# Performance work log

Hardware: AMD Instinct MI355X
Metric: run time of the kernel (lower is better)

Reference implementation:

```python
import jax, jax.numpy as jnp
import numpy as np

N = 50000       # nodes
E = 800000      # directed edges (before self-loops)
IN = 128        # in_channels
H = 8           # heads
C = 32          # hidden_channels (per head)
OUT = 4         # out_channels
NS_ATT = 0.2    # PyG GATConv attention leaky-relu slope
NS_ACT = 0.01   # model activation leaky-relu slope
EPS = 1e-5      # BatchNorm eps


def setup_inputs() -> dict:
    key = jax.random.key(0)
    ks = jax.random.split(key, 18)
    s = 0.05
    return {
        "x": jax.random.normal(ks[0], (N, IN), jnp.float32),
        "edge_index": jax.random.randint(ks[1], (2, E), 0, N, dtype=jnp.int32),
        # layer 1: GATConv(IN -> C, heads=H, concat)
        "W1": jax.random.normal(ks[2], (IN, H * C), jnp.float32) * s,
        "as1": jax.random.normal(ks[3], (H, C), jnp.float32) * s,
        "ad1": jax.random.normal(ks[4], (H, C), jnp.float32) * s,
        "b1": jnp.zeros((H * C,), jnp.float32),
        "g1": jnp.ones((H * C,), jnp.float32),
        "be1": jnp.zeros((H * C,), jnp.float32),
        # middle layer: GATConv(H*C -> C, heads=H, concat) + BN + residual
        "W2": jax.random.normal(ks[5], (H * C, H * C), jnp.float32) * s,
        "as2": jax.random.normal(ks[6], (H, C), jnp.float32) * s,
        "ad2": jax.random.normal(ks[7], (H, C), jnp.float32) * s,
        "b2": jnp.zeros((H * C,), jnp.float32),
        "g2": jnp.ones((H * C,), jnp.float32),
        "be2": jnp.zeros((H * C,), jnp.float32),
        # final layer: GATConv(H*C -> OUT, heads=1, concat=False)
        "W3": jax.random.normal(ks[8], (H * C, OUT), jnp.float32) * s,
        "as3": jax.random.normal(ks[9], (1, OUT), jnp.float32) * s,
        "ad3": jax.random.normal(ks[10], (1, OUT), jnp.float32) * s,
        "b3": jnp.zeros((OUT,), jnp.float32),
    }


def _lrelu(x, slope):
    return jnp.where(x >= 0, x, slope * x)


def _gat_conv(x, src, dst, W, a_src, a_dst, bias, heads, ch, concat):
    # PyG GATConv: h = x @ W per head; edge logit = LReLU(a_src.h_j + a_dst.h_i)
    n = x.shape[0]
    h = (x @ W).reshape(n, heads, ch)                      # [N,H,C]
    al_s = jnp.sum(h * a_src, axis=-1)                     # [N,H]
    al_d = jnp.sum(h * a_dst, axis=-1)                     # [N,H]
    logits = _lrelu(al_s[src] + al_d[dst], NS_ATT)         # [E,H]
    # segment softmax over edges grouped by destination node
    m = jax.ops.segment_max(logits, dst, num_segments=n)   # [N,H]
    e = jnp.exp(logits - m[dst])
    denom = jax.ops.segment_sum(e, dst, num_segments=n)
    alpha = e / (denom[dst] + 1e-16)                       # [E,H]
    out = jax.ops.segment_sum(alpha[:, :, None] * h[src], dst, num_segments=n)  # [N,H,C]
    if concat:
        return out.reshape(n, heads * ch) + bias
    return out.mean(axis=1) + bias


def _bn(x, gamma, beta):
    mu = jnp.mean(x, axis=0)
    var = jnp.mean((x - mu) ** 2, axis=0)
    return (x - mu) * jax.lax.rsqrt(var + EPS) * gamma + beta


def reference(x, edge_index, W1, as1, ad1, b1, g1, be1,
              W2, as2, ad2, b2, g2, be2, W3, as3, ad3, b3):
    n = x.shape[0]
    loops = jnp.arange(n, dtype=edge_index.dtype)          # self-loops (PyG default)
    src = jnp.concatenate([edge_index[0], loops])
    dst = jnp.concatenate([edge_index[1], loops])
    h = _lrelu(_bn(_gat_conv(x, src, dst, W1, as1, ad1, b1, H, C, True), g1, be1), NS_ACT)
    residual = h
    h = _lrelu(_bn(_gat_conv(h, src, dst, W2, as2, ad2, b2, H, C, True), g2, be2), NS_ACT)
    h = h + residual
    return _gat_conv(h, src, dst, W3, as3, ad3, b3, 1, OUT, False)
```

## Files before the change

### kernel.cpp

```cpp
#include <hip/hip_runtime.h>

typedef __attribute__((ext_vector_type(8))) short bf16x8;
typedef __attribute__((ext_vector_type(4))) float f32x4;

__device__ __forceinline__ float lrelu(float x, float s) { return x >= 0.f ? x : s * x; }
__device__ __forceinline__ float b2f(unsigned short u) {
  union { unsigned int i; float f; } v; v.i = ((unsigned int)u) << 16; return v.f;
}
__device__ __forceinline__ float b2f_lo(unsigned int u) {
  union { unsigned int i; float f; } v; v.i = u << 16; return v.f;
}
__device__ __forceinline__ float b2f_hi(unsigned int u) {
  union { unsigned int i; float f; } v; v.i = u & 0xffff0000u; return v.f;
}
__device__ __forceinline__ unsigned short f2b(float f) {
  union { float f; unsigned int i; } v; v.f = f;
  unsigned int r = v.i + 0x7fffu + ((v.i >> 16) & 1u);
  return (unsigned short)(r >> 16);
}
__device__ __forceinline__ unsigned int fbits(float f) {
  union { float f; unsigned int i; } v; v.f = f; return v.i;
}
__device__ __forceinline__ float bitsf(unsigned int u) {
  union { unsigned int i; float f; } v; v.i = u; return v.f;
}

__global__ __launch_bounds__(256) void k_hist(const int* __restrict__ dst, int e,
                                              int* __restrict__ cnt) {
  int i = blockIdx.x * 256 + threadIdx.x;
  if (i < e) atomicAdd(&cnt[dst[i]], 1);
}

__global__ __launch_bounds__(256) void k_bsum(const int* __restrict__ cnt,
                                              int* __restrict__ bsum, int n) {
  const int base = blockIdx.x * 1024;
  const int t = threadIdx.x;
  int s = 0;
#pragma unroll
  for (int i = 0; i < 4; ++i) {
    int idx = base + t + i * 256;
    if (idx < n) s += cnt[idx] + 1;
  }
#pragma unroll
  for (int off = 1; off < 64; off <<= 1) s += __shfl_xor(s, off);
  __shared__ int ws[4];
  const int lane = t & 63, w = t >> 6;
  if (lane == 0) ws[w] = s;
  __syncthreads();
  if (t == 0) bsum[blockIdx.x] = ws[0] + ws[1] + ws[2] + ws[3];
}

__global__ __launch_bounds__(256) void k_scanl(const int* __restrict__ cnt,
                                               const int* __restrict__ bsum,
                                               int* __restrict__ ptr,
                                               int* __restrict__ fill, int n, int B) {
  __shared__ int ws[4];
  __shared__ int bo;
  const int t = threadIdx.x;
  if (t < 64) {
    int v = t < B ? bsum[t] : 0;
    int incl = v;
#pragma unroll
    for (int off = 1; off < 64; off <<= 1) {
      int u = __shfl_up(incl, off);
      if (t >= off) incl += u;
    }
    if (t == blockIdx.x) bo = incl - v;
    if (blockIdx.x == 0 && t == 63) ptr[n] = incl;
  }
  const int base = blockIdx.x * 1024 + t * 4;
  int v0 = base + 0 < n ? cnt[base + 0] + 1 : 0;
  int v1 = base + 1 < n ? cnt[base + 1] + 1 : 0;
  int v2 = base + 2 < n ? cnt[base + 2] + 1 : 0;
  int v3 = base + 3 < n ? cnt[base + 3] + 1 : 0;
  const int tsum = v0 + v1 + v2 + v3;
  const int lane = t & 63, w = t >> 6;
  int incl = tsum;
#pragma unroll
  for (int off = 1; off < 64; off <<= 1) {
    int u = __shfl_up(incl, off);
    if (lane >= off) incl += u;
  }
  if (lane == 63) ws[w] = incl;
  __syncthreads();
  int excl = bo + incl - tsum;
  for (int i = 0; i < w; ++i) excl += ws[i];
  if (base + 0 < n) { ptr[base + 0] = excl; fill[base + 0] = excl; }
  excl += v0;
  if (base + 1 < n) { ptr[base + 1] = excl; fill[base + 1] = excl; }
  excl += v1;
  if (base + 2 < n) { ptr[base + 2] = excl; fill[base + 2] = excl; }
  excl += v2;
  if (base + 3 < n) { ptr[base + 3] = excl; fill[base + 3] = excl; }
}

__global__ __launch_bounds__(256) void k_scatter(const int* __restrict__ srce,
                                                 const int* __restrict__ dste,
                                                 int e, int n,
                                                 int* __restrict__ fill,
                                                 int* __restrict__ srcs) {
  int i = blockIdx.x * 256 + threadIdx.x;
  if (i < e) {
    int pos = atomicAdd(&fill[dste[i]], 1);
    srcs[pos] = srce[i];
  } else if (i < e + n) {
    int v = i - e;
    int pos = atomicAdd(&fill[v], 1);
    srcs[pos] = v;
  }
}

__global__ __launch_bounds__(256) void k_prep(int* __restrict__ cnt, int n,
                                              const float* __restrict__ x,
                                              unsigned short* __restrict__ xb,
                                              const float* __restrict__ W1,
                                              unsigned short* __restrict__ w1t,
                                              const float* __restrict__ W2,
                                              unsigned short* __restrict__ w2t, int n4) {
  int i = blockIdx.x * 256 + threadIdx.x;
  if (i < n) {
    cnt[i] = 0;
  }
  if (i < n) return;
  i -= n;
  if (i < n4) {
    float4 v = ((const float4*)x)[i];
    ushort4 o;
    o.x = f2b(v.x); o.y = f2b(v.y); o.z = f2b(v.z); o.w = f2b(v.w);
    ((ushort4*)xb)[i] = o;
    return;
  }
  i -= n4;
  if (i < 256 * 128) {
    int nn = i / 128, k = i - nn * 128;
    w1t[i] = f2b(W1[(size_t)k * 256 + nn]);
    return;
  }
  i -= 256 * 128;
  if (i < 256 * 256) {
    int nn = i / 256, k = i - nn * 256;
    w2t[i] = f2b(W2[(size_t)k * 256 + nn]);
  }
}

__global__ __launch_bounds__(256) void k_mfma(const unsigned short* __restrict__ A,
                                              const unsigned short* __restrict__ BT,
                                              unsigned short* __restrict__ C,
                                              const float* __restrict__ as_,
                                              const float* __restrict__ ad_,
                                              float* __restrict__ als,
                                              float* __restrict__ ald,
                                              int M, int Nn, int K) {
  __shared__ unsigned int Asu[128 * 20];
  __shared__ unsigned int Bsu[128 * 20];
  const int tid = threadIdx.x;
  const int bm = blockIdx.x * 128, bn = blockIdx.y * 128;
  const int w = tid >> 6, lane = tid & 63;
  const int wm = w >> 1, wn = w & 1;
  const int l16 = lane & 15, lg = lane >> 4;
  f32x4 acc[4][4] = {};
  for (int k0 = 0; k0 < K; k0 += 32) {
#pragma unroll
    for (int rep = 0; rep < 2; ++rep) {
      int ci = tid + rep * 256;
      int row = ci >> 2, cg = ci & 3;
      int ar = bm + row;
      ar = ar < M ? ar : M - 1;
      uint4 av = *(const uint4*)(A + (size_t)ar * K + k0 + cg * 8);
      *(uint4*)&Asu[row * 20 + cg * 4] = av;
      uint4 bv = *(const uint4*)(BT + (size_t)(bn + row) * K + k0 + cg * 8);
      *(uint4*)&Bsu[row * 20 + cg * 4] = bv;
    }
    __syncthreads();
    bf16x8 aF[4], bF[4];
#pragma unroll
    for (int mi = 0; mi < 4; ++mi)
      aF[mi] = *(const bf16x8*)&Asu[(wm * 64 + mi * 16 + l16) * 20 + lg * 4];
#pragma unroll
    for (int ni = 0; ni < 4; ++ni)
      bF[ni] = *(const bf16x8*)&Bsu[(wn * 64 + ni * 16 + l16) * 20 + lg * 4];
#pragma unroll
    for (int mi = 0; mi < 4; ++mi)
#pragma unroll
      for (int ni = 0; ni < 4; ++ni)
        acc[mi][ni] =
            __builtin_amdgcn_mfma_f32_16x16x32_bf16(aF[mi], bF[ni], acc[mi][ni], 0, 0, 0);
    __syncthreads();
  }
  float asv[4], adv[4];
#pragma unroll
  for (int ni = 0; ni < 4; ++ni) {
    int gcol = bn + wn * 64 + ni * 16 + l16;
    asv[ni] = as_[gcol];
    adv[ni] = ad_[gcol];
  }
  const int hb = (bn >> 5) + wn * 2;
#pragma unroll
  for (int mi = 0; mi < 4; ++mi) {
#pragma unroll
    for (int r = 0; r < 4; ++r) {
      int grow = bm + wm * 64 + mi * 16 + lg * 4 + r;
      bool ok = grow < M;
      if (ok) {
#pragma unroll
        for (int ni = 0; ni < 4; ++ni) {
          int gcol = bn + wn * 64 + ni * 16 + l16;
          C[(size_t)grow * Nn + gcol] = f2b(acc[mi][ni][r]);
        }
      }
      float ps0 = acc[mi][0][r] * asv[0] + acc[mi][1][r] * asv[1];
      float ps1 = acc[mi][2][r] * asv[2] + acc[mi][3][r] * asv[3];
      float pd0 = acc[mi][0][r] * adv[0] + acc[mi][1][r] * adv[1];
      float pd1 = acc[mi][2][r] * adv[2] + acc[mi][3][r] * adv[3];
#pragma unroll
      for (int off = 1; off < 16; off <<= 1) {
        ps0 += __shfl_xor(ps0, off);
        ps1 += __shfl_xor(ps1, off);
        pd0 += __shfl_xor(pd0, off);
        pd1 += __shfl_xor(pd1, off);
      }
      if (ok && l16 == 0) {
        *(float2*)(als + (size_t)grow * 8 + hb) = make_float2(ps0, ps1);
        *(float2*)(ald + (size_t)grow * 8 + hb) = make_float2(pd0, pd1);
      }
    }
  }
}

__global__ __launch_bounds__(256) void k_agg(const unsigned short* __restrict__ h,
                                             const float* __restrict__ als,
                                             const float* __restrict__ ald,
                                             const int* __restrict__ ptr,
                                             const int* __restrict__ srcs,
                                             const float* __restrict__ bias,
                                             unsigned short* __restrict__ out, int n) {
  int wid = (blockIdx.x * 256 + threadIdx.x) >> 6;
  int lane = threadIdx.x & 63;
  if (wid >= n) return;
  const int beg = ptr[wid], end = ptr[wid + 1];
  const int L = lane & 15;
  const int e = lane >> 4;
  const int hh = L >> 1;
  const float adh = ald[(size_t)wid * 8 + hh];
  float s = 0.f;
  float a0 = 0, a1 = 0, a2 = 0, a3 = 0, a4 = 0, a5 = 0, a6 = 0, a7 = 0;
  float a8 = 0, a9 = 0, aA = 0, aB = 0, aC = 0, aD = 0, aE = 0, aF = 0;
  for (int j = beg + e; j < end; j += 8) {
    const int jB = j + 4;
    const bool vB = jB < end;
    int sA = srcs[j];
    int sB = vB ? srcs[jB] : sA;
    const uint4* hpA = (const uint4*)(h + (size_t)sA * 256 + L * 16);
    const uint4* hpB = (const uint4*)(h + (size_t)sB * 256 + L * 16);
    uint4 cA0 = hpA[0];
    uint4 cA1 = hpA[1];
    uint4 cB0 = hpB[0];
    uint4 cB1 = hpB[1];
    float alsA = als[(size_t)sA * 8 + hh];
    float alsB = als[(size_t)sB * 8 + hh];
    float wtA = __expf(lrelu(alsA + adh, 0.2f));
    s += wtA;
    a0 += wtA * b2f_lo(cA0.x); a1 += wtA * b2f_hi(cA0.x);
    a2 += wtA * b2f_lo(cA0.y); a3 += wtA * b2f_hi(cA0.y);
    a4 += wtA * b2f_lo(cA0.z); a5 += wtA * b2f_hi(cA0.z);
    a6 += wtA * b2f_lo(cA0.w); a7 += wtA * b2f_hi(cA0.w);
    a8 += wtA * b2f_lo(cA1.x); a9 += wtA * b2f_hi(cA1.x);
    aA += wtA * b2f_lo(cA1.y); aB += wtA * b2f_hi(cA1.y);
    aC += wtA * b2f_lo(cA1.z); aD += wtA * b2f_hi(cA1.z);
    aE += wtA * b2f_lo(cA1.w); aF += wtA * b2f_hi(cA1.w);
    float wtB = vB ? __expf(lrelu(alsB + adh, 0.2f)) : 0.f;
    s += wtB;
    a0 += wtB * b2f_lo(cB0.x); a1 += wtB * b2f_hi(cB0.x);
    a2 += wtB * b2f_lo(cB0.y); a3 += wtB * b2f_hi(cB0.y);
    a4 += wtB * b2f_lo(cB0.z); a5 += wtB * b2f_hi(cB0.z);
    a6 += wtB * b2f_lo(cB0.w); a7 += wtB * b2f_hi(cB0.w);
    a8 += wtB * b2f_lo(cB1.x); a9 += wtB * b2f_hi(cB1.x);
    aA += wtB * b2f_lo(cB1.y); aB += wtB * b2f_hi(cB1.y);
    aC += wtB * b2f_lo(cB1.z); aD += wtB * b2f_hi(cB1.z);
    aE += wtB * b2f_lo(cB1.w); aF += wtB * b2f_hi(cB1.w);
  }
  a0 += __shfl_xor(a0, 16); a0 += __shfl_xor(a0, 32);
  a1 += __shfl_xor(a1, 16); a1 += __shfl_xor(a1, 32);
  a2 += __shfl_xor(a2, 16); a2 += __shfl_xor(a2, 32);
  a3 += __shfl_xor(a3, 16); a3 += __shfl_xor(a3, 32);
  a4 += __shfl_xor(a4, 16); a4 += __shfl_xor(a4, 32);
  a5 += __shfl_xor(a5, 16); a5 += __shfl_xor(a5, 32);
  a6 += __shfl_xor(a6, 16); a6 += __shfl_xor(a6, 32);
  a7 += __shfl_xor(a7, 16); a7 += __shfl_xor(a7, 32);
  a8 += __shfl_xor(a8, 16); a8 += __shfl_xor(a8, 32);
  a9 += __shfl_xor(a9, 16); a9 += __shfl_xor(a9, 32);
  aA += __shfl_xor(aA, 16); aA += __shfl_xor(aA, 32);
  aB += __shfl_xor(aB, 16); aB += __shfl_xor(aB, 32);
  aC += __shfl_xor(aC, 16); aC += __shfl_xor(aC, 32);
  aD += __shfl_xor(aD, 16); aD += __shfl_xor(aD, 32);
  aE += __shfl_xor(aE, 16); aE += __shfl_xor(aE, 32);
  aF += __shfl_xor(aF, 16); aF += __shfl_xor(aF, 32);
  s += __shfl_xor(s, 16); s += __shfl_xor(s, 32);
  const float inv = 1.f / (s + 1e-16f);
  if (e == 0) {
    const float4* bp = (const float4*)(bias + L * 16);
    float4 b0 = bp[0], b1 = bp[1], b2 = bp[2], b3 = bp[3];
    uint4 o0, o1;
    o0.x = (unsigned int)f2b(a0 * inv + b0.x) | ((unsigned int)f2b(a1 * inv + b0.y) << 16);
    o0.y = (unsigned int)f2b(a2 * inv + b0.z) | ((unsigned int)f2b(a3 * inv + b0.w) << 16);
    o0.z = (unsigned int)f2b(a4 * inv + b1.x) | ((unsigned int)f2b(a5 * inv + b1.y) << 16);
    o0.w = (unsigned int)f2b(a6 * inv + b1.z) | ((unsigned int)f2b(a7 * inv + b1.w) << 16);
    o1.x = (unsigned int)f2b(a8 * inv + b2.x) | ((unsigned int)f2b(a9 * inv + b2.y) << 16);
    o1.y = (unsigned int)f2b(aA * inv + b2.z) | ((unsigned int)f2b(aB * inv + b2.w) << 16);
    o1.z = (unsigned int)f2b(aC * inv + b3.x) | ((unsigned int)f2b(aD * inv + b3.y) << 16);
    o1.w = (unsigned int)f2b(aE * inv + b3.z) | ((unsigned int)f2b(aF * inv + b3.w) << 16);
    uint4* op = (uint4*)(out + (size_t)wid * 256 + L * 16);
    op[0] = o0;
    op[1] = o1;
  }
}

__global__ __launch_bounds__(256) void k_bnp1(const unsigned short* __restrict__ x,
                                              float* __restrict__ partial, int n) {
  const int t = threadIdx.x;
  const int q = t & 63;
  const int rsub = t >> 6;
  float s0 = 0, s1 = 0, s2 = 0, s3 = 0, q0 = 0, q1 = 0, q2 = 0, q3 = 0;
  int r = blockIdx.x * 4 + rsub;
  for (; r + 6144 < n; r += 8192) {
    ushort4 va = *(const ushort4*)(x + (size_t)r * 256 + q * 4);
    ushort4 vb = *(const ushort4*)(x + (size_t)(r + 2048) * 256 + q * 4);
    ushort4 vc = *(const ushort4*)(x + (size_t)(r + 4096) * 256 + q * 4);
    ushort4 vd = *(const ushort4*)(x + (size_t)(r + 6144) * 256 + q * 4);
    float f;
    f = b2f(va.x); s0 += f; q0 += f * f;
    f = b2f(va.y); s1 += f; q1 += f * f;
    f = b2f(va.z); s2 += f; q2 += f * f;
    f = b2f(va.w); s3 += f; q3 += f * f;
    f = b2f(vb.x); s0 += f; q0 += f * f;
    f = b2f(vb.y); s1 += f; q1 += f * f;
    f = b2f(vb.z); s2 += f; q2 += f * f;
    f = b2f(vb.w); s3 += f; q3 += f * f;
    f = b2f(vc.x); s0 += f; q0 += f * f;
    f = b2f(vc.y); s1 += f; q1 += f * f;
    f = b2f(vc.z); s2 += f; q2 += f * f;
    f = b2f(vc.w); s3 += f; q3 += f * f;
    f = b2f(vd.x); s0 += f; q0 += f * f;
    f = b2f(vd.y); s1 += f; q1 += f * f;
    f = b2f(vd.z); s2 += f; q2 += f * f;
    f = b2f(vd.w); s3 += f; q3 += f * f;
  }
  for (; r < n; r += 2048) {
    ushort4 v = *(const ushort4*)(x + (size_t)r * 256 + q * 4);
    float f;
    f = b2f(v.x); s0 += f; q0 += f * f;
    f = b2f(v.y); s1 += f; q1 += f * f;
    f = b2f(v.z); s2 += f; q2 += f * f;
    f = b2f(v.w); s3 += f; q3 += f * f;
  }
  __shared__ float ls[4][512];
  ls[rsub][q * 4 + 0] = s0; ls[rsub][q * 4 + 1] = s1;
  ls[rsub][q * 4 + 2] = s2; ls[rsub][q * 4 + 3] = s3;
  ls[rsub][256 + q * 4 + 0] = q0; ls[rsub][256 + q * 4 + 1] = q1;
  ls[rsub][256 + q * 4 + 2] = q2; ls[rsub][256 + q * 4 + 3] = q3;
  __syncthreads();
  float a = ls[0][t] + ls[1][t] + ls[2][t] + ls[3][t];
  float b = ls[0][256 + t] + ls[1][256 + t] + ls[2][256 + t] + ls[3][256 + t];
  partial[blockIdx.x * 512 + t] = a;
  partial[blockIdx.x * 512 + 256 + t] = b;
}

__global__ __launch_bounds__(256) void k_bnp2(const float* __restrict__ partial,
                                              const float* __restrict__ ga,
                                              const float* __restrict__ be,
                                              float* __restrict__ ss, float invn) {
  const int c = blockIdx.x * 4 + (threadIdx.x >> 6);
  const int lane = threadIdx.x & 63;
  float s = 0.f, qq = 0.f;
#pragma unroll
  for (int k = 0; k < 8; ++k) {
    int b = lane + k * 64;
    s += partial[(size_t)b * 512 + c];
    qq += partial[(size_t)b * 512 + 256 + c];
  }
#pragma unroll
  for (int off = 1; off < 64; off <<= 1) {
    s += __shfl_xor(s, off);
    qq += __shfl_xor(qq, off);
  }
  if (lane == 0) {
    float mu = s * invn;
    float var = qq * invn - mu * mu;
    float sc = ga[c] * rsqrtf(var + 1e-5f);
    ss[c] = sc;
    ss[256 + c] = be[c] - mu * sc;
  }
}

__global__ __launch_bounds__(256) void k_bnact(const unsigned short* __restrict__ x,
                                               const float* __restrict__ ss,
                                               unsigned short* __restrict__ out, int n) {
  const int tot4 = n * 64;
  for (int t = blockIdx.x * 256 + threadIdx.x; t < tot4; t += gridDim.x * 256) {
    int i0 = t * 4;
    int c = i0 & 255;
    ushort4 xu = *(const ushort4*)(x + i0);
    float4 scv = *(const float4*)(ss + c);
    float4 shv = *(const float4*)(ss + 256 + c);
    float t0 = b2f(xu.x) * scv.x + shv.x;
    float t1 = b2f(xu.y) * scv.y + shv.y;
    float t2 = b2f(xu.z) * scv.z + shv.z;
    float t3 = b2f(xu.w) * scv.w + shv.w;
    float o0 = fmaxf(t0, 0.01f * t0);
    float o1 = fmaxf(t1, 0.01f * t1);
    float o2 = fmaxf(t2, 0.01f * t2);
    float o3 = fmaxf(t3, 0.01f * t3);
    ushort4 ob;
    ob.x = f2b(o0); ob.y = f2b(o1); ob.z = f2b(o2); ob.w = f2b(o3);
    *(ushort4*)(out + i0) = ob;
  }
}

__global__ __launch_bounds__(256) void k_bnact3(const unsigned short* __restrict__ x,
                                                const float* __restrict__ ss,
                                                const unsigned short* __restrict__ res,
                                                const float* __restrict__ W3,
                                                const float* __restrict__ as3,
                                                const float* __restrict__ ad3,
                                                uint4* __restrict__ h3p, int n) {
  int wid = (blockIdx.x * 256 + threadIdx.x) >> 6;
  int lane = threadIdx.x & 63;
  if (wid >= n) return;
  const int c = lane * 4;
  ushort4 xu = *(const ushort4*)(x + (size_t)wid * 256 + c);
  ushort4 rv = *(const ushort4*)(res + (size_t)wid * 256 + c);
  float4 scv = *(const float4*)(ss + c);
  float4 shv = *(const float4*)(ss + 256 + c);
  float t0 = b2f(xu.x) * scv.x + shv.x;
  float t1 = b2f(xu.y) * scv.y + shv.y;
  float t2 = b2f(xu.z) * scv.z + shv.z;
  float t3 = b2f(xu.w) * scv.w + shv.w;
  float o0 = fmaxf(t0, 0.01f * t0) + b2f(rv.x);
  float o1 = fmaxf(t1, 0.01f * t1) + b2f(rv.y);
  float o2 = fmaxf(t2, 0.01f * t2) + b2f(rv.z);
  float o3 = fmaxf(t3, 0.01f * t3) + b2f(rv.w);
  const float4* Wp = (const float4*)W3 + lane * 4;
  float4 w0 = Wp[0], w1 = Wp[1], w2 = Wp[2], w3 = Wp[3];
  float a0 = o0 * w0.x + o1 * w1.x + o2 * w2.x + o3 * w3.x;
  float a1 = o0 * w0.y + o1 * w1.y + o2 * w2.y + o3 * w3.y;
  float a2 = o0 * w0.z + o1 * w1.z + o2 * w2.z + o3 * w3.z;
  float a3 = o0 * w0.w + o1 * w1.w + o2 * w2.w + o3 * w3.w;
#pragma unroll
  for (int off = 1; off < 64; off <<= 1) {
    a0 += __shfl_xor(a0, off);
    a1 += __shfl_xor(a1, off);
    a2 += __shfl_xor(a2, off);
    a3 += __shfl_xor(a3, off);
  }
  if (lane == 0) {
    float als3v = a0 * as3[0] + a1 * as3[1] + a2 * as3[2] + a3 * as3[3];
    float ald3v = a0 * ad3[0] + a1 * ad3[1] + a2 * ad3[2] + a3 * ad3[3];
    uint4 pv;
    pv.x = (unsigned int)f2b(a0) | ((unsigned int)f2b(a1) << 16);
    pv.y = (unsigned int)f2b(a2) | ((unsigned int)f2b(a3) << 16);
    pv.z = fbits(als3v);
    pv.w = fbits(ald3v);
    h3p[wid] = pv;
  }
}

__global__ __launch_bounds__(256) void k_agg3(const uint4* __restrict__ h3p,
                                              const int* __restrict__ ptr,
                                              const int* __restrict__ srcs,
                                              const float* __restrict__ b3,
                                              float* __restrict__ out, int n) {
  int wid = (blockIdx.x * 256 + threadIdx.x) >> 6;
  int lane = threadIdx.x & 63;
  if (wid >= n) return;
  const int beg = ptr[wid], end = ptr[wid + 1];
  const float aldh = bitsf(h3p[wid].w);
  float s = 0.f, a0 = 0.f, a1 = 0.f, a2 = 0.f, a3 = 0.f;
  for (int j = beg + lane; j < end; j += 64) {
    uint4 v = h3p[srcs[j]];
    float wgt = __expf(lrelu(bitsf(v.z) + aldh, 0.2f));
    s += wgt;
    a0 += wgt * b2f_lo(v.x);
    a1 += wgt * b2f_hi(v.x);
    a2 += wgt * b2f_lo(v.y);
    a3 += wgt * b2f_hi(v.y);
  }
#pragma unroll
  for (int off = 1; off < 64; off <<= 1) {
    s += __shfl_xor(s, off);
    a0 += __shfl_xor(a0, off);
    a1 += __shfl_xor(a1, off);
    a2 += __shfl_xor(a2, off);
    a3 += __shfl_xor(a3, off);
  }
  if (lane == 0) {
    float inv = 1.f / (s + 1e-16f);
    out[(size_t)wid * 4 + 0] = a0 * inv + b3[0];
    out[(size_t)wid * 4 + 1] = a1 * inv + b3[1];
    out[(size_t)wid * 4 + 2] = a2 * inv + b3[2];
    out[(size_t)wid * 4 + 3] = a3 * inv + b3[3];
  }
}

extern "C" void kernel_launch(void* const* d_in, const int* in_sizes, int n_in,
                              void* d_out, int out_size, void* d_ws, size_t ws_size,
                              hipStream_t stream) {
  const float* x   = (const float*)d_in[0];
  const int*   ei  = (const int*)d_in[1];
  const float* W1  = (const float*)d_in[2];
  const float* as1 = (const float*)d_in[3];
  const float* ad1 = (const float*)d_in[4];
  const float* b1  = (const float*)d_in[5];
  const float* ga1 = (const float*)d_in[6];
  const float* be1 = (const float*)d_in[7];
  const float* W2  = (const float*)d_in[8];
  const float* as2 = (const float*)d_in[9];
  const float* ad2 = (const float*)d_in[10];
  const float* b2  = (const float*)d_in[11];
  const float* ga2 = (const float*)d_in[12];
  const float* be2 = (const float*)d_in[13];
  const float* W3  = (const float*)d_in[14];
  const float* as3 = (const float*)d_in[15];
  const float* ad3 = (const float*)d_in[16];
  const float* b3  = (const float*)d_in[17];

  const int N = in_sizes[0] / 128;
  const int E = in_sizes[1] / 2;
  const int ET = E + N;
  float* out = (float*)d_out;

  char* w = (char*)d_ws;
  auto alloc = [&](size_t bytes) -> void* {
    void* p = (void*)w;
    w += (bytes + 255) & ~(size_t)255;
    return p;
  };
  int* ptr              = (int*)alloc((size_t)(N + 1) * 4);
  int* fill             = (int*)alloc((size_t)N * 4);
  int* cnt              = (int*)alloc((size_t)N * 4);
  int* bsum             = (int*)alloc(64 * 4);
  int* srcs             = (int*)alloc((size_t)ET * 4);
  unsigned short* hbuf  = (unsigned short*)alloc((size_t)N * 256 * 2);
  unsigned short* aggb  = (unsigned short*)alloc((size_t)N * 256 * 2);
  unsigned short* a1b   = (unsigned short*)alloc((size_t)N * 256 * 2);
  unsigned short* xb    = (unsigned short*)alloc((size_t)N * 128 * 2);
  unsigned short* w1t   = (unsigned short*)alloc(256 * 128 * 2);
  unsigned short* w2t   = (unsigned short*)alloc(256 * 256 * 2);
  float* als            = (float*)alloc((size_t)N * 8 * 4);
  float* ald            = (float*)alloc((size_t)N * 8 * 4);
  uint4* h3p            = (uint4*)alloc((size_t)N * 16);
  float* partial        = (float*)alloc(512 * 512 * 4);
  float* ss             = (float*)alloc(1024 * 4);

  const int* esrc = ei;
  const int* edst = ei + E;
  const float invn = 1.f / (float)N;

  const int n4 = N * 32;
  const int prep_tot = N + n4 + 256 * 128 + 256 * 256;
  k_prep<<<(prep_tot + 255) / 256, 256, 0, stream>>>(cnt, N, x, xb, W1, w1t, W2, w2t, n4);

  const int B = (N + 1023) / 1024;
  k_hist<<<(E + 255) / 256, 256, 0, stream>>>(edst, E, cnt);
  k_bsum<<<B, 256, 0, stream>>>(cnt, bsum, N);
  k_scanl<<<B, 256, 0, stream>>>(cnt, bsum, ptr, fill, N, B);
  k_scatter<<<(ET + 255) / 256, 256, 0, stream>>>(esrc, edst, E, N, fill, srcs);

  const dim3 gemm_grid((N + 127) / 128, 2);
  const int wblocks = (N + 3) / 4;

  k_mfma<<<gemm_grid, 256, 0, stream>>>(xb, w1t, hbuf, as1, ad1, als, ald, N, 256, 128);
  k_agg<<<wblocks, 256, 0, stream>>>(hbuf, als, ald, ptr, srcs, b1, aggb, N);
  k_bnp1<<<512, 256, 0, stream>>>(aggb, partial, N);
  k_bnp2<<<64, 256, 0, stream>>>(partial, ga1, be1, ss, invn);
  k_bnact<<<2048, 256, 0, stream>>>(aggb, ss, a1b, N);

  k_mfma<<<gemm_grid, 256, 0, stream>>>(a1b, w2t, hbuf, as2, ad2, als, ald, N, 256, 256);
  k_agg<<<wblocks, 256, 0, stream>>>(hbuf, als, ald, ptr, srcs, b2, aggb, N);
  k_bnp1<<<512, 256, 0, stream>>>(aggb, partial, N);
  k_bnp2<<<64, 256, 0, stream>>>(partial, ga2, be2, ss + 512, invn);
  k_bnact3<<<wblocks, 256, 0, stream>>>(aggb, ss + 512, a1b, W3, as3, ad3, h3p, N);

  k_agg3<<<wblocks, 256, 0, stream>>>(h3p, ptr, srcs, b3, out, N);
}
```

Baseline: 374.5 us.

## Restructure GAT aggregation to per-head persistent waves with 16 edges in flight

Rewrites the aggregation kernel so that each block handles a single attention head, and a wave loops persistently over destination nodes on a fixed 2048-block grid. Each lane covers 8 channels of one head, and 16 edges are processed in parallel per wave, in place of 4 edge groups covering all 256 channels. This is meant to raise memory-level parallelism for the gathered neighbour rows and to cut per-lane register pressure. The cost is that srcs/ptr/ald are re-read once per head, and each gather is only 64 bytes per edge per head. Separately, the edge-scatter writes and the srcs loads now use nontemporal hints, and the prep kernel's divisions become shifts and masks.

```diff
diff --git a/kernel.cpp b/kernel.cpp
--- a/kernel.cpp
+++ b/kernel.cpp
@@ -102,11 +102,11 @@
   int i = blockIdx.x * 256 + threadIdx.x;
   if (i < e) {
     int pos = atomicAdd(&fill[dste[i]], 1);
-    srcs[pos] = srce[i];
+    __builtin_nontemporal_store(srce[i], &srcs[pos]);
   } else if (i < e + n) {
     int v = i - e;
     int pos = atomicAdd(&fill[v], 1);
-    srcs[pos] = v;
+    __builtin_nontemporal_store(v, &srcs[pos]);
   }
 }
 
@@ -120,8 +120,8 @@
   int i = blockIdx.x * 256 + threadIdx.x;
   if (i < n) {
     cnt[i] = 0;
-  }
-  if (i < n) return;
+    return;
+  }
   i -= n;
   if (i < n4) {
     float4 v = ((const float4*)x)[i];
@@ -132,13 +132,13 @@
   }
   i -= n4;
   if (i < 256 * 128) {
-    int nn = i / 128, k = i - nn * 128;
+    int nn = i >> 7, k = i & 127;
     w1t[i] = f2b(W1[(size_t)k * 256 + nn]);
     return;
   }
   i -= 256 * 128;
   if (i < 256 * 256) {
-    int nn = i / 256, k = i - nn * 256;
+    int nn = i >> 8, k = i & 255;
     w2t[i] = f2b(W2[(size_t)k * 256 + nn]);
   }
 }
@@ -234,84 +234,52 @@
                                              const int* __restrict__ srcs,
                                              const float* __restrict__ bias,
                                              unsigned short* __restrict__ out, int n) {
-  int wid = (blockIdx.x * 256 + threadIdx.x) >> 6;
-  int lane = threadIdx.x & 63;
-  if (wid >= n) return;
-  const int beg = ptr[wid], end = ptr[wid + 1];
-  const int L = lane & 15;
-  const int e = lane >> 4;
-  const int hh = L >> 1;
-  const float adh = ald[(size_t)wid * 8 + hh];
-  float s = 0.f;
-  float a0 = 0, a1 = 0, a2 = 0, a3 = 0, a4 = 0, a5 = 0, a6 = 0, a7 = 0;
-  float a8 = 0, a9 = 0, aA = 0, aB = 0, aC = 0, aD = 0, aE = 0, aF = 0;
-  for (int j = beg + e; j < end; j += 8) {
-    const int jB = j + 4;
-    const bool vB = jB < end;
-    int sA = srcs[j];
-    int sB = vB ? srcs[jB] : sA;
-    const uint4* hpA = (const uint4*)(h + (size_t)sA * 256 + L * 16);
-    const uint4* hpB = (const uint4*)(h + (size_t)sB * 256 + L * 16);
-    uint4 cA0 = hpA[0];
-    uint4 cA1 = hpA[1];
-    uint4 cB0 = hpB[0];
-    uint4 cB1 = hpB[1];
-    float alsA = als[(size_t)sA * 8 + hh];
-    float alsB = als[(size_t)sB * 8 + hh];
-    float wtA = __expf(lrelu(alsA + adh, 0.2f));
-    s += wtA;
-    a0 += wtA * b2f_lo(cA0.x); a1 += wtA * b2f_hi(cA0.x);
-    a2 += wtA * b2f_lo(cA0.y); a3 += wtA * b2f_hi(cA0.y);
-    a4 += wtA * b2f_lo(cA0.z); a5 += wtA * b2f_hi(cA0.z);
-    a6 += wtA * b2f_lo(cA0.w); a7 += wtA * b2f_hi(cA0.w);
-    a8 += wtA * b2f_lo(cA1.x); a9 += wtA * b2f_hi(cA1.x);
-    aA += wtA * b2f_lo(cA1.y); aB += wtA * b2f_hi(cA1.y);
-    aC += wtA * b2f_lo(cA1.z); aD += wtA * b2f_hi(cA1.z);
-    aE += wtA * b2f_lo(cA1.w); aF += wtA * b2f_hi(cA1.w);
-    float wtB = vB ? __expf(lrelu(alsB + adh, 0.2f)) : 0.f;
-    s += wtB;
-    a0 += wtB * b2f_lo(cB0.x); a1 += wtB * b2f_hi(cB0.x);
-    a2 += wtB * b2f_lo(cB0.y); a3 += wtB * b2f_hi(cB0.y);
-    a4 += wtB * b2f_lo(cB0.z); a5 += wtB * b2f_hi(cB0.z);
-    a6 += wtB * b2f_lo(cB0.w); a7 += wtB * b2f_hi(cB0.w);
-    a8 += wtB * b2f_lo(cB1.x); a9 += wtB * b2f_hi(cB1.x);
-    aA += wtB * b2f_lo(cB1.y); aB += wtB * b2f_hi(cB1.y);
-    aC += wtB * b2f_lo(cB1.z); aD += wtB * b2f_hi(cB1.z);
-    aE += wtB * b2f_lo(cB1.w); aF += wtB * b2f_hi(cB1.w);
-  }
-  a0 += __shfl_xor(a0, 16); a0 += __shfl_xor(a0, 32);
-  a1 += __shfl_xor(a1, 16); a1 += __shfl_xor(a1, 32);
-  a2 += __shfl_xor(a2, 16); a2 += __shfl_xor(a2, 32);
-  a3 += __shfl_xor(a3, 16); a3 += __shfl_xor(a3, 32);
-  a4 += __shfl_xor(a4, 16); a4 += __shfl_xor(a4, 32);
-  a5 += __shfl_xor(a5, 16); a5 += __shfl_xor(a5, 32);
-  a6 += __shfl_xor(a6, 16); a6 += __shfl_xor(a6, 32);
-  a7 += __shfl_xor(a7, 16); a7 += __shfl_xor(a7, 32);
-  a8 += __shfl_xor(a8, 16); a8 += __shfl_xor(a8, 32);
-  a9 += __shfl_xor(a9, 16); a9 += __shfl_xor(a9, 32);
-  aA += __shfl_xor(aA, 16); aA += __shfl_xor(aA, 32);
-  aB += __shfl_xor(aB, 16); aB += __shfl_xor(aB, 32);
-  aC += __shfl_xor(aC, 16); aC += __shfl_xor(aC, 32);
-  aD += __shfl_xor(aD, 16); aD += __shfl_xor(aD, 32);
-  aE += __shfl_xor(aE, 16); aE += __shfl_xor(aE, 32);
-  aF += __shfl_xor(aF, 16); aF += __shfl_xor(aF, 32);
-  s += __shfl_xor(s, 16); s += __shfl_xor(s, 32);
-  const float inv = 1.f / (s + 1e-16f);
-  if (e == 0) {
-    const float4* bp = (const float4*)(bias + L * 16);
-    float4 b0 = bp[0], b1 = bp[1], b2 = bp[2], b3 = bp[3];
-    uint4 o0, o1;
-    o0.x = (unsigned int)f2b(a0 * inv + b0.x) | ((unsigned int)f2b(a1 * inv + b0.y) << 16);
-    o0.y = (unsigned int)f2b(a2 * inv + b0.z) | ((unsigned int)f2b(a3 * inv + b0.w) << 16);
-    o0.z = (unsigned int)f2b(a4 * inv + b1.x) | ((unsigned int)f2b(a5 * inv + b1.y) << 16);
-    o0.w = (unsigned int)f2b(a6 * inv + b1.z) | ((unsigned int)f2b(a7 * inv + b1.w) << 16);
-    o1.x = (unsigned int)f2b(a8 * inv + b2.x) | ((unsigned int)f2b(a9 * inv + b2.y) << 16);
-    o1.y = (unsigned int)f2b(aA * inv + b2.z) | ((unsigned int)f2b(aB * inv + b2.w) << 16);
-    o1.z = (unsigned int)f2b(aC * inv + b3.x) | ((unsigned int)f2b(aD * inv + b3.y) << 16);
-    o1.w = (unsigned int)f2b(aE * inv + b3.z) | ((unsigned int)f2b(aF * inv + b3.w) << 16);
-    uint4* op = (uint4*)(out + (size_t)wid * 256 + L * 16);
-    op[0] = o0;
-    op[1] = o1;
+  const int head = blockIdx.x & 7;
+  const int wv = threadIdx.x >> 6;
+  const int lane = threadIdx.x & 63;
+  const int e = lane >> 2;
+  const int l = lane & 3;
+  const int ch = head * 32 + l * 8;
+  const float4 bv0 = *(const float4*)(bias + ch);
+  const float4 bv1 = *(const float4*)(bias + ch + 4);
+  const int dst0 = (blockIdx.x >> 3) * 4 + wv;
+  const int dstep = (gridDim.x >> 3) * 4;
+  for (int dst = dst0; dst < n; dst += dstep) {
+    const int beg = ptr[dst], end = ptr[dst + 1];
+    const float adh = ald[(size_t)dst * 8 + head];
+    float s = 0.f;
+    float a0 = 0, a1 = 0, a2 = 0, a3 = 0, a4 = 0, a5 = 0, a6 = 0, a7 = 0;
+    for (int j = beg + e; j < end; j += 16) {
+      int src = __builtin_nontemporal_load(&srcs[j]);
+      float wt = __expf(lrelu(als[(size_t)src * 8 + head] + adh, 0.2f));
+      uint4 hv = *(const uint4*)(h + (size_t)src * 256 + ch);
+      s += wt;
+      a0 += wt * b2f_lo(hv.x); a1 += wt * b2f_hi(hv.x);
+      a2 += wt * b2f_lo(hv.y); a3 += wt * b2f_hi(hv.y);
+      a4 += wt * b2f_lo(hv.z); a5 += wt * b2f_hi(hv.z);
+      a6 += wt * b2f_lo(hv.w); a7 += wt * b2f_hi(hv.w);
+    }
+#pragma unroll
+    for (int off = 4; off < 64; off <<= 1) {
+      s  += __shfl_xor(s, off);
+      a0 += __shfl_xor(a0, off);
+      a1 += __shfl_xor(a1, off);
+      a2 += __shfl_xor(a2, off);
+      a3 += __shfl_xor(a3, off);
+      a4 += __shfl_xor(a4, off);
+      a5 += __shfl_xor(a5, off);
+      a6 += __shfl_xor(a6, off);
+      a7 += __shfl_xor(a7, off);
+    }
+    if (e == 0) {
+      float inv = 1.f / (s + 1e-16f);
+      uint4 o;
+      o.x = (unsigned int)f2b(a0 * inv + bv0.x) | ((unsigned int)f2b(a1 * inv + bv0.y) << 16);
+      o.y = (unsigned int)f2b(a2 * inv + bv0.z) | ((unsigned int)f2b(a3 * inv + bv0.w) << 16);
+      o.z = (unsigned int)f2b(a4 * inv + bv1.x) | ((unsigned int)f2b(a5 * inv + bv1.y) << 16);
+      o.w = (unsigned int)f2b(a6 * inv + bv1.z) | ((unsigned int)f2b(a7 * inv + bv1.w) << 16);
+      *(uint4*)(out + (size_t)dst * 256 + ch) = o;
+    }
   }
 }
 
@@ -567,15 +535,16 @@
 
   const dim3 gemm_grid((N + 127) / 128, 2);
   const int wblocks = (N + 3) / 4;
+  const int agg_grid = 2048;
 
   k_mfma<<<gemm_grid, 256, 0, stream>>>(xb, w1t, hbuf, as1, ad1, als, ald, N, 256, 128);
-  k_agg<<<wblocks, 256, 0, stream>>>(hbuf, als, ald, ptr, srcs, b1, aggb, N);
+  k_agg<<<agg_grid, 256, 0, stream>>>(hbuf, als, ald, ptr, srcs, b1, aggb, N);
   k_bnp1<<<512, 256, 0, stream>>>(aggb, partial, N);
   k_bnp2<<<64, 256, 0, stream>>>(partial, ga1, be1, ss, invn);
   k_bnact<<<2048, 256, 0, stream>>>(aggb, ss, a1b, N);
 
   k_mfma<<<gemm_grid, 256, 0, stream>>>(a1b, w2t, hbuf, as2, ad2, als, ald, N, 256, 256);
-  k_agg<<<wblocks, 256, 0, stream>>>(hbuf, als, ald, ptr, srcs, b2, aggb, N);
+  k_agg<<<agg_grid, 256, 0, stream>>>(hbuf, als, ald, ptr, srcs, b2, aggb, N);
   k_bnp1<<<512, 256, 0, stream>>>(aggb, partial, N);
   k_bnp2<<<64, 256, 0, stream>>>(partial, ga2, be2, ss + 512, invn);
   k_bnact3<<<wblocks, 256, 0, stream>>>(aggb, ss + 512, a1b, W3, as3, ad3, h3p, N);
```

Result: slower. 613.7 us (+63.9%).
